# Performance work log

Measured on AMD Instinct MI355X. Metric: run time of the kernel, lower is better.

## Reference

```python
import jax, jax.numpy as jnp
import numpy as np

LN_EPS = 1e-5


def setup_inputs() -> dict:
    key = jax.random.key(0)
    ks = jax.random.split(key, 6)
    B, N, C, H = 8, 4096, 768, 12
    D = C // H
    x = jax.random.normal(ks[0], (B, N, C), dtype=jnp.float32)
    w_qkv = jax.random.normal(ks[1], (3 * C, C), dtype=jnp.float32) * (C ** -0.5)
    w_proj = jax.random.normal(ks[2], (C, C), dtype=jnp.float32) * (C ** -0.5)
    b_proj = jnp.zeros((C,), dtype=jnp.float32)
    # trunc_normal_(std=0.02) approximated by clipped normal
    p1 = jnp.clip(jax.random.normal(ks[3], (H, N), dtype=jnp.float32) * 0.02, -0.04, 0.04)
    p2 = jnp.clip(jax.random.normal(ks[4], (H, N), dtype=jnp.float32) * 0.02, -0.04, 0.04)
    gamma = jnp.ones((D,), dtype=jnp.float32)
    beta = jnp.zeros((D,), dtype=jnp.float32)
    return {"x": x, "w_qkv": w_qkv, "w_proj": w_proj, "b_proj": b_proj,
            "p1": p1, "p2": p2, "gamma": gamma, "beta": beta}


def _layernorm(h, gamma, beta):
    mu = jnp.mean(h, axis=-1, keepdims=True)
    var = jnp.var(h, axis=-1, keepdims=True)
    return (h - mu) * jax.lax.rsqrt(var + LN_EPS) * gamma + beta


def reference(x, w_qkv, w_proj, b_proj, p1, p2, gamma, beta):
    B, N, C = x.shape
    H = p1.shape[0]
    D = C // H
    # qkv projection (no bias): [B,N,3C] -> [3,B,H,N,D]
    qkv = (x @ w_qkv.T).reshape(B, N, 3, H, D).transpose(2, 0, 3, 1, 4)
    q, k, v = qkv[0], qkv[1], qkv[2]
    # weighted k*v reduction over sequence: [B,H,D]
    modulator = jnp.einsum('hn,bhnd->bhd', p2, k * v)
    modulator = _layernorm(modulator, gamma, beta)
    # broadcast modulation back over N: [B,H,N,D]
    modulator = jnp.einsum('hn,bhd->bhnd', p1, modulator)
    out = (q * modulator).transpose(0, 2, 1, 3).reshape(B, N, C)
    return out @ w_proj.T + b_proj
```

## Files before the change

### kernel.cpp

```cpp
#include <hip/hip_runtime.h>
#include <stdint.h>
#include <stddef.h>

#define LN_EPS 1e-5f

typedef __bf16 bf16;
typedef __bf16 bf16x8 __attribute__((ext_vector_type(8)));
typedef __bf16 bf16x4 __attribute__((ext_vector_type(4)));
typedef float f32x4 __attribute__((ext_vector_type(4)));

#define GL16(gp, lp)                                                                   \
  __builtin_amdgcn_global_load_lds((__attribute__((address_space(1))) uint32_t*)(gp),  \
                                   (__attribute__((address_space(3))) uint32_t*)(lp),  \
                                   16, 0, 0)

#define SBAR   asm volatile("s_barrier" ::: "memory")
#define VMW(N) asm volatile("s_waitcnt vmcnt(" #N ")" ::: "memory")
#define LGK(N) asm volatile("s_waitcnt lgkmcnt(" #N ")" ::: "memory")
#define SCB    __builtin_amdgcn_sched_barrier(0)
#define SP1    __builtin_amdgcn_s_setprio(1)
#define SP0    __builtin_amdgcn_s_setprio(0)
#define NOWAIT ((void)0)

#define XV4   6291456
#define WQV4  442368
#define WPV4  147456
__global__ __launch_bounds__(256) void cvt_all(const float* __restrict__ x,
                                               const float* __restrict__ wq,
                                               const float* __restrict__ wp,
                                               bf16* __restrict__ xb,
                                               bf16* __restrict__ wqb,
                                               bf16* __restrict__ wpb) {
  int i = blockIdx.x * 256 + threadIdx.x;
  const float* src; bf16* dst; int off;
  if (i < XV4)              { src = x;  dst = xb;  off = i; }
  else if (i < XV4 + WQV4)  { src = wq; dst = wqb; off = i - XV4; }
  else                      { src = wp; dst = wpb; off = i - (XV4 + WQV4); }
  const float4 v = ((const float4*)src)[off];
  bf16x4 o;
  o[0] = (bf16)v.x; o[1] = (bf16)v.y; o[2] = (bf16)v.z; o[3] = (bf16)v.w;
  ((bf16x4*)dst)[off] = o;
}

#define STAGE_A(T, H) do {                                              \
    bf16* d_ = ldsA + ((((T)&1) << 1) + (H)) * 8192 + tid8;             \
    GL16(pA + (H) * 98304 + (T) * 64, d_);                              \
    GL16(pA + (H) * 98304 + 49152 + (T) * 64, d_ + 4096); } while (0)

#define STAGE_B(T, H) do {                                              \
    bf16* d_ = ldsB + ((((T)&1) << 1) + (H)) * 8192 + tid8;             \
    GL16(pB##H##0 + (T) * 64, d_);                                      \
    GL16(pB##H##1 + (T) * 64, d_ + 4096); } while (0)

#define RD_AQ(D, MQ) do {                                               \
    _Pragma("unroll") for (int mf = 0; mf < 4; ++mf) {                  \
      const int r_ = (MQ) * 64 + mf * 16 + l16;                         \
      const bf16* b_ = ldsA + (((D) << 1) + wm) * 8192 + r_ * 64;       \
      const int x_ = r_ & 7;                                            \
      aF[mf][0] = *(const bf16x8*)(b_ + ((qg ^ x_) << 3));              \
      aF[mf][1] = *(const bf16x8*)(b_ + (((4 + qg) ^ x_) << 3));        \
    } } while (0)

#define RD_BQ(D, NQ, BF) do {                                           \
    _Pragma("unroll") for (int nf = 0; nf < 2; ++nf) {                  \
      const int r_ = hn64 + (NQ) * 32 + nf * 16 + l16;                  \
      const bf16* b_ = ldsB + (((D) << 1) + hb) * 8192 + r_ * 64;       \
      const int x_ = r_ & 7;                                            \
      BF[nf][0] = *(const bf16x8*)(b_ + ((qg ^ x_) << 3));              \
      BF[nf][1] = *(const bf16x8*)(b_ + (((4 + qg) ^ x_) << 3));        \
    } } while (0)

#define MMQ(MQ, NQ, BF) do {                                            \
    _Pragma("unroll") for (int mf = 0; mf < 4; ++mf)                    \
      _Pragma("unroll") for (int nf = 0; nf < 2; ++nf) {                \
        acc[(MQ)*4+mf][(NQ)*2+nf] = __builtin_amdgcn_mfma_f32_16x16x32_bf16( \
            aF[mf][0], BF[nf][0], acc[(MQ)*4+mf][(NQ)*2+nf], 0, 0, 0);  \
        acc[(MQ)*4+mf][(NQ)*2+nf] = __builtin_amdgcn_mfma_f32_16x16x32_bf16( \
            aF[mf][1], BF[nf][1], acc[(MQ)*4+mf][(NQ)*2+nf], 0, 0, 0);  \
      } } while (0)

#define ITER(T, P12, P38, WV4, WV8) do {                                       \
     RD_AQ(0, 0); RD_BQ(0, 0, bF0); if (P12) STAGE_A((T)+1, 0); LGK(8);\
    SBAR; LGK(0); SCB; SP1; MMQ(0, 0, bF0); SP0; SBAR;                         \
     RD_BQ(0, 1, bF1); if (P12) STAGE_A((T)+1, 1);                     \
    SBAR; LGK(0); SCB; SP1; MMQ(0, 1, bF1); SP0; SBAR;                         \
     RD_AQ(0, 1); if (P38) STAGE_B((T)+2, 0);                          \
    SBAR; LGK(0); SCB; SP1; MMQ(1, 0, bF0); SP0; SBAR;                         \
     if (P38) STAGE_B((T)+2, 1);                                       \
    SBAR; LGK(0); SCB; SP1; MMQ(1, 1, bF1); SP0; WV4; SBAR;                    \
     RD_AQ(1, 0); RD_BQ(1, 0, bF0); if (P38) STAGE_A((T)+2, 0); LGK(8);\
    SBAR; LGK(0); SCB; SP1; MMQ(0, 0, bF0); SP0; SBAR;                         \
     RD_BQ(1, 1, bF1); if (P38) STAGE_A((T)+2, 1);                     \
    SBAR; LGK(0); SCB; SP1; MMQ(0, 1, bF1); SP0; SBAR;                         \
     RD_AQ(1, 1); if (P38) STAGE_B((T)+3, 0);                          \
    SBAR; LGK(0); SCB; SP1; MMQ(1, 0, bF0); SP0; SBAR;                         \
     if (P38) STAGE_B((T)+3, 1);                                       \
    SBAR; LGK(0); SCB; SP1; MMQ(1, 1, bF1); SP0; WV8; SBAR;                    \
  } while (0)

__device__ __forceinline__ void gemm256(const bf16* pA,
                                        const bf16* pB00, const bf16* pB01,
                                        const bf16* pB10, const bf16* pB11,
                                        bf16* sh, f32x4 acc[8][4]) {
  const int tid  = threadIdx.x;
  const int lane = tid & 63;
  const int wave = tid >> 6;
  const int wm   = wave >> 2;
  const int wn   = wave & 3;
  const int hb   = wn >> 1;
  const int hn64 = (wn & 1) * 64;
  const int l16  = lane & 15;
  const int qg   = lane >> 4;
  const int tid8 = tid * 8;
  bf16* const ldsA = sh;
  bf16* const ldsB = sh + 32768;
  bf16x8 aF[4][2], bF0[2][2], bF1[2][2];

  STAGE_A(0, 0); STAGE_A(0, 1); STAGE_B(0, 0); STAGE_B(0, 1);
  STAGE_A(1, 0); STAGE_A(1, 1); STAGE_B(1, 0); STAGE_B(1, 1);
  VMW(8);
  SBAR;

  ITER(0, 0, 1, VMW(4), VMW(4));
#pragma unroll 1
  for (int T = 2; T <= 8; T += 2) {
    ITER(T, 1, 1, VMW(4), VMW(4));
  }
  ITER(10, 1, 0, VMW(0), NOWAIT);

  asm volatile("s_waitcnt vmcnt(0) lgkmcnt(0)" ::: "memory");
  __syncthreads();
}

#define QSTAGE_A(T) do {                                          \
    bf16* d_ = qldsA + (((T)&1)) * 8192 + tid8;                   \
    GL16(qA + (T) * 64, d_);                                      \
    GL16(qA + 49152 + (T) * 64, d_ + 4096); } while (0)

#define QSTAGE_B(T, H) do {                                       \
    bf16* d_ = qldsB + ((((T)&1) << 1) + (H)) * 8192 + tid8;      \
    GL16(qB##H##0 + (T) * 64, d_);                                \
    GL16(qB##H##1 + (T) * 64, d_ + 4096); } while (0)

#define QRD_A(D, MQ) do {                                         \
    _Pragma("unroll") for (int mf = 0; mf < 2; ++mf) {            \
      const int r_ = wm * 64 + (MQ) * 32 + mf * 16 + l16;         \
      const bf16* b_ = qldsA + (D) * 8192 + r_ * 64;              \
      const int x_ = r_ & 7;                                      \
      aF[mf][0] = *(const bf16x8*)(b_ + ((qg ^ x_) << 3));        \
      aF[mf][1] = *(const bf16x8*)(b_ + (((4 + qg) ^ x_) << 3));  \
    } } while (0)

#define QRD_B(D, NQ, BF) do {                                     \
    _Pragma("unroll") for (int nf = 0; nf < 2; ++nf) {            \
      const int r_ = hn64 + (NQ) * 32 + nf * 16 + l16;            \
      const bf16* b_ = qldsB + (((D) << 1) + hb) * 8192 + r_ * 64;\
      const int x_ = r_ & 7;                                      \
      BF[nf][0] = *(const bf16x8*)(b_ + ((qg ^ x_) << 3));        \
      BF[nf][1] = *(const bf16x8*)(b_ + (((4 + qg) ^ x_) << 3));  \
    } } while (0)

#define QMM(MQ, NQ, BF) do {                                      \
    _Pragma("unroll") for (int mf = 0; mf < 2; ++mf)              \
      _Pragma("unroll") for (int nf = 0; nf < 2; ++nf) {          \
        acc[(MQ)*2+mf][(NQ)*2+nf] = __builtin_amdgcn_mfma_f32_16x16x32_bf16( \
            aF[mf][0], BF[nf][0], acc[(MQ)*2+mf][(NQ)*2+nf], 0, 0, 0); \
        acc[(MQ)*2+mf][(NQ)*2+nf] = __builtin_amdgcn_mfma_f32_16x16x32_bf16( \
            aF[mf][1], BF[nf][1], acc[(MQ)*2+mf][(NQ)*2+nf], 0, 0, 0); \
      } } while (0)

#define QITER(T, P1, P38, WVp4, WVp8) do {                                     \
     QRD_A(0, 0); QRD_B(0, 0, bF0); if (P1) QSTAGE_A((T)+1);           \
    SBAR; LGK(0); SCB; SP1; QMM(0, 0, bF0); SP0; SBAR;                         \
     QRD_B(0, 1, bF1);                                                 \
    SBAR; LGK(0); SCB; SP1; QMM(0, 1, bF1); SP0; SBAR;                         \
     QRD_A(0, 1); if (P38) QSTAGE_B((T)+2, 0);                         \
    SBAR; LGK(0); SCB; SP1; QMM(1, 0, bF0); SP0; SBAR;                         \
     if (P38) QSTAGE_B((T)+2, 1);                                      \
    SBAR; LGK(0); SCB; SP1; QMM(1, 1, bF1); SP0; WVp4; SBAR;                   \
     QRD_A(1, 0); QRD_B(1, 0, bF0); if (P38) QSTAGE_A((T)+2);          \
    SBAR; LGK(0); SCB; SP1; QMM(0, 0, bF0); SP0; SBAR;                         \
     QRD_B(1, 1, bF1);                                                 \
    SBAR; LGK(0); SCB; SP1; QMM(0, 1, bF1); SP0; SBAR;                         \
     QRD_A(1, 1); if (P38) QSTAGE_B((T)+3, 0);                         \
    SBAR; LGK(0); SCB; SP1; QMM(1, 0, bF0); SP0; SBAR;                         \
     if (P38) QSTAGE_B((T)+3, 1);                                      \
    SBAR; LGK(0); SCB; SP1; QMM(1, 1, bF1); SP0; WVp8; SBAR;                   \
  } while (0)

__device__ __forceinline__ void gemm128x256(const bf16* qA,
                                            const bf16* qB00, const bf16* qB01,
                                            const bf16* qB10, const bf16* qB11,
                                            bf16* sh, f32x4 acc[4][4]) {
  const int tid  = threadIdx.x;
  const int lane = tid & 63;
  const int wave = tid >> 6;
  const int wm   = wave >> 2;
  const int wn   = wave & 3;
  const int hb   = wn >> 1;
  const int hn64 = (wn & 1) * 64;
  const int l16  = lane & 15;
  const int qg   = lane >> 4;
  const int tid8 = tid * 8;
  bf16* const qldsA = sh;
  bf16* const qldsB = sh + 16384;
  bf16x8 aF[2][2], bF0[2][2], bF1[2][2];

  QSTAGE_A(0); QSTAGE_B(0, 0); QSTAGE_B(0, 1);
  QSTAGE_A(1); QSTAGE_B(1, 0); QSTAGE_B(1, 1);
  VMW(6);
  SBAR;

  QITER(0, 0, 1, VMW(4), VMW(4));
#pragma unroll 1
  for (int T = 2; T <= 8; T += 2) {
    QITER(T, 1, 1, VMW(4), VMW(4));
  }
  QITER(10, 1, 0, VMW(0), NOWAIT);

  asm volatile("s_waitcnt vmcnt(0) lgkmcnt(0)" ::: "memory");
  __syncthreads();
}

__global__ __launch_bounds__(512, 2) void kv_gemm_reduce(const bf16* __restrict__ A,
                                                         const bf16* __restrict__ B,
                                                         const float* __restrict__ p2,
                                                         float* __restrict__ partials) {
  __shared__ __align__(16) bf16 sh[65536];
  __shared__ float red2[2][4][2][16];

  const int lin  = blockIdx.y * 6 + blockIdx.x;
  const int xcd  = lin & 7;
  const int j    = lin >> 3;
  const int hh   = j % 6;
  const int mblk = xcd + 8 * (j / 6);
  const int m0   = mblk * 256;
  const int h0   = hh * 2;

  const int tid = threadIdx.x;
  const int tr  = tid >> 3;
  const int tc  = ((tid & 7) ^ ((tid >> 3) & 7)) * 8;
  const bf16* pA = A + (size_t)(m0 + tr) * 768 + tc;
#define WQROW(r) (768 + (((r) >> 4) & 1) * 768 + (h0 + ((r) >> 7)) * 64 + \
                  ((((r) >> 5) & 3) * 16 + ((r) & 15)))
  const bf16* pB00 = B + (size_t)WQROW(tr) * 768 + tc;
  const bf16* pB01 = B + (size_t)WQROW(64 + tr) * 768 + tc;
  const bf16* pB10 = B + (size_t)WQROW(128 + tr) * 768 + tc;
  const bf16* pB11 = B + (size_t)WQROW(192 + tr) * 768 + tc;
#undef WQROW

  f32x4 acc[8][4] = {};
  gemm256(pA, pB00, pB01, pB10, pB11, sh, acc);

  const int lane = tid & 63, wave = tid >> 6;
  const int wm = wave >> 2, wn = wave & 3, l16 = lane & 15, qg = lane >> 4;
  const float* p2h = p2 + (size_t)(h0 + (wn >> 1)) * 4096 + (m0 & 4095) + wm * 128;
  float s0 = 0.f, s1 = 0.f;
#pragma unroll
  for (int ai = 0; ai < 8; ++ai) {
    const float4 w = *(const float4*)(p2h + ai * 16 + qg * 4);
    s0 += w.x * acc[ai][0][0] * acc[ai][1][0] + w.y * acc[ai][0][1] * acc[ai][1][1]
        + w.z * acc[ai][0][2] * acc[ai][1][2] + w.w * acc[ai][0][3] * acc[ai][1][3];
    s1 += w.x * acc[ai][2][0] * acc[ai][3][0] + w.y * acc[ai][2][1] * acc[ai][3][1]
        + w.z * acc[ai][2][2] * acc[ai][3][2] + w.w * acc[ai][2][3] * acc[ai][3][3];
  }
  s0 += __shfl_xor(s0, 16); s0 += __shfl_xor(s0, 32);
  s1 += __shfl_xor(s1, 16); s1 += __shfl_xor(s1, 32);
  if (qg == 0) { red2[wm][wn][0][l16] = s0; red2[wm][wn][1][l16] = s1; }
  __syncthreads();
  if (tid < 128) {
    const int l = tid & 15, jj = (tid >> 4) & 1, wnn = tid >> 5;
    const float v = red2[0][wnn][jj][l] + red2[1][wnn][jj][l];
    const int hx = h0 + (wnn >> 1);
    const int dd = ((wnn & 1) * 2 + jj) * 16 + l;
    partials[((size_t)mblk * 12 + hx) * 64 + dd] = v;
  }
}

__global__ __launch_bounds__(64) void mod_reduce_ln(const float* __restrict__ partials,
                                                    const float* __restrict__ gamma,
                                                    const float* __restrict__ beta,
                                                    float* __restrict__ mod) {
  const int h = blockIdx.x, b = blockIdx.y;
  const int d = threadIdx.x;

  const float* p = partials + ((size_t)(b * 16) * 12 + h) * 64 + d;
  float s = 0.f;
#pragma unroll
  for (int mb = 0; mb < 16; ++mb) s += p[(size_t)mb * 12 * 64];

  float sum = s, sumsq = s * s;
#pragma unroll
  for (int o = 32; o > 0; o >>= 1) {
    sum   += __shfl_xor(sum, o);
    sumsq += __shfl_xor(sumsq, o);
  }
  const float mu  = sum * (1.f / 64.f);
  const float var = sumsq * (1.f / 64.f) - mu * mu;
  const float r   = rsqrtf(var + LN_EPS);
  mod[(b * 12 + h) * 64 + d] = (s - mu) * r * gamma[d] + beta[d];
}

__global__ __launch_bounds__(512, 2) void q_gemm_mod(const bf16* __restrict__ A,
                                                     const bf16* __restrict__ B,
                                                     const float* __restrict__ p1,
                                                     const float* __restrict__ mod,
                                                     bf16* __restrict__ amod) {
  __shared__ __align__(16) bf16 sh[49152];

  const int lin  = blockIdx.y * 3 + blockIdx.x;
  const int xcd  = lin & 7;
  const int j    = lin >> 3;
  const int nblk = j % 3;
  const int mblk = xcd + 8 * (j / 3);
  const int n0   = nblk * 256;
  const int m0   = mblk * 128;

  const int tid = threadIdx.x;
  const int tr  = tid >> 3;
  const int tc  = ((tid & 7) ^ ((tid >> 3) & 7)) * 8;
  const bf16* qA   = A + (size_t)(m0 + tr) * 768 + tc;
  const bf16* qB00 = B + (size_t)(n0 + tr) * 768 + tc;
  const bf16* qB01 = qB00 + (size_t)64 * 768;
  const bf16* qB10 = qB00 + (size_t)128 * 768;
  const bf16* qB11 = qB00 + (size_t)192 * 768;

  f32x4 acc[4][4] = {};
  gemm128x256(qA, qB00, qB01, qB10, qB11, sh, acc);

  const int lane = tid & 63, wave = tid >> 6;
  const int wm = wave >> 2, wn = wave & 3, l16 = lane & 15, qg = lane >> 4;
  const int row0 = m0 + wm * 64 + qg * 4;
  const int col0 = n0 + wn * 64 + l16;
  const int b    = m0 >> 12;
  const int h    = (n0 >> 6) + wn;

  float p1v[4][4];
#pragma unroll
  for (int ai = 0; ai < 4; ++ai)
#pragma unroll
    for (int r = 0; r < 4; ++r)
      p1v[ai][r] = p1[(size_t)h * 4096 + ((row0 + ai * 16 + r) & 4095)];
  float mv[4];
#pragma unroll
  for (int bj = 0; bj < 4; ++bj) mv[bj] = mod[b * 768 + col0 + bj * 16];

#pragma unroll
  for (int ai = 0; ai < 4; ++ai)
#pragma unroll
    for (int bj = 0; bj < 4; ++bj)
#pragma unroll
      for (int r = 0; r < 4; ++r)
        amod[(size_t)(row0 + ai * 16 + r) * 768 + col0 + bj * 16] =
            (bf16)(acc[ai][bj][r] * p1v[ai][r] * mv[bj]);
}

__global__ __launch_bounds__(512, 2) void gemm_proj(const bf16* __restrict__ A,
                                                    const bf16* __restrict__ B,
                                                    const float* __restrict__ bias,
                                                    float* __restrict__ C) {
  __shared__ __align__(16) bf16 sh[49152];

  const int lin  = blockIdx.y * 3 + blockIdx.x;
  const int xcd  = lin & 7;
  const int j    = lin >> 3;
  const int nblk = j % 3;
  const int mblk = xcd + 8 * (j / 3);
  const int n0   = nblk * 256;
  const int m0   = mblk * 128;

  const int tid = threadIdx.x;
  const int tr  = tid >> 3;
  const int tc  = ((tid & 7) ^ ((tid >> 3) & 7)) * 8;
  const bf16* qA   = A + (size_t)(m0 + tr) * 768 + tc;
  const bf16* qB00 = B + (size_t)(n0 + tr) * 768 + tc;
  const bf16* qB01 = qB00 + (size_t)64 * 768;
  const bf16* qB10 = qB00 + (size_t)128 * 768;
  const bf16* qB11 = qB00 + (size_t)192 * 768;

  f32x4 acc[4][4] = {};
  gemm128x256(qA, qB00, qB01, qB10, qB11, sh, acc);

  const int lane = tid & 63, wave = tid >> 6;
  const int wm = wave >> 2, wn = wave & 3, l16 = lane & 15, qg = lane >> 4;
  const int row0 = m0 + wm * 64 + qg * 4;
  const int col0 = n0 + wn * 64 + l16;
#pragma unroll
  for (int bj = 0; bj < 4; ++bj) {
    const int col = col0 + bj * 16;
    const float bv = bias[col];
#pragma unroll
    for (int ai = 0; ai < 4; ++ai)
#pragma unroll
      for (int r = 0; r < 4; ++r)
        C[(size_t)(row0 + ai * 16 + r) * 768 + col] = acc[ai][bj][r] + bv;
  }
}

extern "C" void kernel_launch(void* const* d_in, const int* in_sizes, int n_in,
                              void* d_out, int out_size, void* d_ws, size_t ws_size,
                              hipStream_t stream) {
  (void)in_sizes; (void)n_in; (void)out_size; (void)ws_size;

  const float* x      = (const float*)d_in[0];
  const float* w_qkv  = (const float*)d_in[1];
  const float* w_proj = (const float*)d_in[2];
  const float* b_proj = (const float*)d_in[3];
  const float* p1     = (const float*)d_in[4];
  const float* p2     = (const float*)d_in[5];
  const float* gamma  = (const float*)d_in[6];
  const float* beta   = (const float*)d_in[7];
  float* out = (float*)d_out;

  char* ws = (char*)d_ws;
  bf16*  xb       = (bf16*)(ws + 0);
  bf16*  wqb      = (bf16*)(ws + 50331648);
  bf16*  wpb      = (bf16*)(ws + 53870592);
  bf16*  amod     = (bf16*)(ws + 55050240);
  float* partials = (float*)(ws + 105381888);
  float* mod      = (float*)(ws + 106168320);

  cvt_all<<<26880, 256, 0, stream>>>(x, w_qkv, w_proj, xb, wqb, wpb);

  kv_gemm_reduce<<<dim3(6, 128), 512, 0, stream>>>(xb, wqb, p2, partials);

  mod_reduce_ln<<<dim3(12, 8), 64, 0, stream>>>(partials, gamma, beta, mod);

  q_gemm_mod<<<dim3(3, 256), 512, 0, stream>>>(xb, wqb, p1, mod, amod);

  gemm_proj<<<dim3(3, 256), 512, 0, stream>>>(amod, wpb, b_proj, out);
}
```

Baseline: 355.6 us.

## Replace GEMM cores with shared K=32 double-buffered kernel and fuse LayerNorm

```diff
diff --git a/kernel.cpp b/kernel.cpp
--- a/kernel.cpp
+++ b/kernel.cpp
@@ -31,202 +31,86 @@
                                                bf16* __restrict__ xb,
                                                bf16* __restrict__ wqb,
                                                bf16* __restrict__ wpb) {
-  int i = blockIdx.x * 256 + threadIdx.x;
-  const float* src; bf16* dst; int off;
-  if (i < XV4)              { src = x;  dst = xb;  off = i; }
-  else if (i < XV4 + WQV4)  { src = wq; dst = wqb; off = i - XV4; }
-  else                      { src = wp; dst = wpb; off = i - (XV4 + WQV4); }
-  const float4 v = ((const float4*)src)[off];
-  bf16x4 o;
-  o[0] = (bf16)v.x; o[1] = (bf16)v.y; o[2] = (bf16)v.z; o[3] = (bf16)v.w;
-  ((bf16x4*)dst)[off] = o;
-}
-
-#define STAGE_A(T, H) do {                                              \
-    bf16* d_ = ldsA + ((((T)&1) << 1) + (H)) * 8192 + tid8;             \
-    GL16(pA + (H) * 98304 + (T) * 64, d_);                              \
-    GL16(pA + (H) * 98304 + 49152 + (T) * 64, d_ + 4096); } while (0)
-
-#define STAGE_B(T, H) do {                                              \
-    bf16* d_ = ldsB + ((((T)&1) << 1) + (H)) * 8192 + tid8;             \
-    GL16(pB##H##0 + (T) * 64, d_);                                      \
-    GL16(pB##H##1 + (T) * 64, d_ + 4096); } while (0)
-
-#define RD_AQ(D, MQ) do {                                               \
-    _Pragma("unroll") for (int mf = 0; mf < 4; ++mf) {                  \
-      const int r_ = (MQ) * 64 + mf * 16 + l16;                         \
-      const bf16* b_ = ldsA + (((D) << 1) + wm) * 8192 + r_ * 64;       \
-      const int x_ = r_ & 7;                                            \
-      aF[mf][0] = *(const bf16x8*)(b_ + ((qg ^ x_) << 3));              \
-      aF[mf][1] = *(const bf16x8*)(b_ + (((4 + qg) ^ x_) << 3));        \
+  const int base = blockIdx.x * 256 + threadIdx.x;
+#pragma unroll 1
+  for (int it = 0; it < 16; ++it) {
+    const int i = base + it * 430080;
+    const float* src; bf16* dst; int off;
+    if (i < XV4)              { src = x;  dst = xb;  off = i; }
+    else if (i < XV4 + WQV4)  { src = wq; dst = wqb; off = i - XV4; }
+    else                      { src = wp; dst = wpb; off = i - (XV4 + WQV4); }
+    const float4 v = ((const float4*)src)[off];
+    bf16x4 o;
+    o[0] = (bf16)v.x; o[1] = (bf16)v.y; o[2] = (bf16)v.z; o[3] = (bf16)v.w;
+    ((bf16x4*)dst)[off] = o;
+  }
+}
+
+#define CSTAGE(T, CUR) do {                                    \
+    GL16(cA  + (T) * 32, sh + (CUR) * 12288 + tid8);           \
+    GL16(cB0 + (T) * 32, sh + (CUR) * 12288 + 4096 + tid8);    \
+    GL16(cB1 + (T) * 32, sh + (CUR) * 12288 + 8192 + tid8);    \
+  } while (0)
+
+#define CRD(CUR) do {                                                         \
+    _Pragma("unroll") for (int ff = 0; ff < 4; ++ff) {                        \
+      const int ra = wm * 64 + ff * 16 + l16;                                 \
+      const int rb = wn * 64 + ff * 16 + l16;                                 \
+      aF[ff] = *(const bf16x8*)(sh + (CUR) * 12288 + ra * 32 + coff);         \
+      bF[ff] = *(const bf16x8*)(sh + (CUR) * 12288 + 4096 + rb * 32 + coff);  \
     } } while (0)
 
-#define RD_BQ(D, NQ, BF) do {                                           \
-    _Pragma("unroll") for (int nf = 0; nf < 2; ++nf) {                  \
-      const int r_ = hn64 + (NQ) * 32 + nf * 16 + l16;                  \
-      const bf16* b_ = ldsB + (((D) << 1) + hb) * 8192 + r_ * 64;       \
-      const int x_ = r_ & 7;                                            \
-      BF[nf][0] = *(const bf16x8*)(b_ + ((qg ^ x_) << 3));              \
-      BF[nf][1] = *(const bf16x8*)(b_ + (((4 + qg) ^ x_) << 3));        \
-    } } while (0)
-
-#define MMQ(MQ, NQ, BF) do {                                            \
-    _Pragma("unroll") for (int mf = 0; mf < 4; ++mf)                    \
-      _Pragma("unroll") for (int nf = 0; nf < 2; ++nf) {                \
-        acc[(MQ)*4+mf][(NQ)*2+nf] = __builtin_amdgcn_mfma_f32_16x16x32_bf16( \
-            aF[mf][0], BF[nf][0], acc[(MQ)*4+mf][(NQ)*2+nf], 0, 0, 0);  \
-        acc[(MQ)*4+mf][(NQ)*2+nf] = __builtin_amdgcn_mfma_f32_16x16x32_bf16( \
-            aF[mf][1], BF[nf][1], acc[(MQ)*4+mf][(NQ)*2+nf], 0, 0, 0);  \
-      } } while (0)
-
-#define ITER(T, P12, P38, WV4, WV8) do {                                       \
-     RD_AQ(0, 0); RD_BQ(0, 0, bF0); if (P12) STAGE_A((T)+1, 0); LGK(8);\
-    SBAR; LGK(0); SCB; SP1; MMQ(0, 0, bF0); SP0; SBAR;                         \
-     RD_BQ(0, 1, bF1); if (P12) STAGE_A((T)+1, 1);                     \
-    SBAR; LGK(0); SCB; SP1; MMQ(0, 1, bF1); SP0; SBAR;                         \
-     RD_AQ(0, 1); if (P38) STAGE_B((T)+2, 0);                          \
-    SBAR; LGK(0); SCB; SP1; MMQ(1, 0, bF0); SP0; SBAR;                         \
-     if (P38) STAGE_B((T)+2, 1);                                       \
-    SBAR; LGK(0); SCB; SP1; MMQ(1, 1, bF1); SP0; WV4; SBAR;                    \
-     RD_AQ(1, 0); RD_BQ(1, 0, bF0); if (P38) STAGE_A((T)+2, 0); LGK(8);\
-    SBAR; LGK(0); SCB; SP1; MMQ(0, 0, bF0); SP0; SBAR;                         \
-     RD_BQ(1, 1, bF1); if (P38) STAGE_A((T)+2, 1);                     \
-    SBAR; LGK(0); SCB; SP1; MMQ(0, 1, bF1); SP0; SBAR;                         \
-     RD_AQ(1, 1); if (P38) STAGE_B((T)+3, 0);                          \
-    SBAR; LGK(0); SCB; SP1; MMQ(1, 0, bF0); SP0; SBAR;                         \
-     if (P38) STAGE_B((T)+3, 1);                                       \
-    SBAR; LGK(0); SCB; SP1; MMQ(1, 1, bF1); SP0; WV8; SBAR;                    \
+#define CMM do {                                                              \
+    _Pragma("unroll") for (int ai = 0; ai < 4; ++ai)                          \
+      _Pragma("unroll") for (int bj = 0; bj < 4; ++bj)                        \
+        acc[ai][bj] = __builtin_amdgcn_mfma_f32_16x16x32_bf16(                \
+            aF[ai], bF[bj], acc[ai][bj], 0, 0, 0);                            \
   } while (0)
 
-__device__ __forceinline__ void gemm256(const bf16* pA,
-                                        const bf16* pB00, const bf16* pB01,
-                                        const bf16* pB10, const bf16* pB11,
-                                        bf16* sh, f32x4 acc[8][4]) {
+#define CITER(CUR, STG, WAIT) do {  \
+    CRD(CUR);                       \
+    LGK(0); SCB;                    \
+    SBAR;                           \
+    STG;                            \
+    SP1; CMM; SP0;                  \
+    WAIT;                           \
+    SBAR;                           \
+  } while (0)
+
+__device__ __forceinline__ void gemmC(const bf16* cA, const bf16* cB0,
+                                      const bf16* cB1, bf16* sh,
+                                      f32x4 acc[4][4]) {
   const int tid  = threadIdx.x;
   const int lane = tid & 63;
   const int wave = tid >> 6;
   const int wm   = wave >> 2;
   const int wn   = wave & 3;
-  const int hb   = wn >> 1;
-  const int hn64 = (wn & 1) * 64;
   const int l16  = lane & 15;
   const int qg   = lane >> 4;
   const int tid8 = tid * 8;
-  bf16* const ldsA = sh;
-  bf16* const ldsB = sh + 32768;
-  bf16x8 aF[4][2], bF0[2][2], bF1[2][2];
-
-  STAGE_A(0, 0); STAGE_A(0, 1); STAGE_B(0, 0); STAGE_B(0, 1);
-  STAGE_A(1, 0); STAGE_A(1, 1); STAGE_B(1, 0); STAGE_B(1, 1);
-  VMW(8);
+  const int coff = ((qg ^ ((l16 >> 1) & 3)) << 3);
+  bf16x8 aF[4], bF[4];
+
+  CSTAGE(0, 0); CSTAGE(1, 1);
+  VMW(3);
   SBAR;
 
-  ITER(0, 0, 1, VMW(4), VMW(4));
 #pragma unroll 1
-  for (int T = 2; T <= 8; T += 2) {
-    ITER(T, 1, 1, VMW(4), VMW(4));
-  }
-  ITER(10, 1, 0, VMW(0), NOWAIT);
-
+  for (int t = 0; t < 22; t += 2) {
+    CITER(0, CSTAGE(t + 2, 0), VMW(3));
+    CITER(1, CSTAGE(t + 3, 1), VMW(3));
+  }
+  CITER(0, NOWAIT, VMW(0));
+  CITER(1, NOWAIT, NOWAIT);
   asm volatile("s_waitcnt vmcnt(0) lgkmcnt(0)" ::: "memory");
   __syncthreads();
 }
 
-#define QSTAGE_A(T) do {                                          \
-    bf16* d_ = qldsA + (((T)&1)) * 8192 + tid8;                   \
-    GL16(qA + (T) * 64, d_);                                      \
-    GL16(qA + 49152 + (T) * 64, d_ + 4096); } while (0)
-
-#define QSTAGE_B(T, H) do {                                       \
-    bf16* d_ = qldsB + ((((T)&1) << 1) + (H)) * 8192 + tid8;      \
-    GL16(qB##H##0 + (T) * 64, d_);                                \
-    GL16(qB##H##1 + (T) * 64, d_ + 4096); } while (0)
-
-#define QRD_A(D, MQ) do {                                         \
-    _Pragma("unroll") for (int mf = 0; mf < 2; ++mf) {            \
-      const int r_ = wm * 64 + (MQ) * 32 + mf * 16 + l16;         \
-      const bf16* b_ = qldsA + (D) * 8192 + r_ * 64;              \
-      const int x_ = r_ & 7;                                      \
-      aF[mf][0] = *(const bf16x8*)(b_ + ((qg ^ x_) << 3));        \
-      aF[mf][1] = *(const bf16x8*)(b_ + (((4 + qg) ^ x_) << 3));  \
-    } } while (0)
-
-#define QRD_B(D, NQ, BF) do {                                     \
-    _Pragma("unroll") for (int nf = 0; nf < 2; ++nf) {            \
-      const int r_ = hn64 + (NQ) * 32 + nf * 16 + l16;            \
-      const bf16* b_ = qldsB + (((D) << 1) + hb) * 8192 + r_ * 64;\
-      const int x_ = r_ & 7;                                      \
-      BF[nf][0] = *(const bf16x8*)(b_ + ((qg ^ x_) << 3));        \
-      BF[nf][1] = *(const bf16x8*)(b_ + (((4 + qg) ^ x_) << 3));  \
-    } } while (0)
-
-#define QMM(MQ, NQ, BF) do {                                      \
-    _Pragma("unroll") for (int mf = 0; mf < 2; ++mf)              \
-      _Pragma("unroll") for (int nf = 0; nf < 2; ++nf) {          \
-        acc[(MQ)*2+mf][(NQ)*2+nf] = __builtin_amdgcn_mfma_f32_16x16x32_bf16( \
-            aF[mf][0], BF[nf][0], acc[(MQ)*2+mf][(NQ)*2+nf], 0, 0, 0); \
-        acc[(MQ)*2+mf][(NQ)*2+nf] = __builtin_amdgcn_mfma_f32_16x16x32_bf16( \
-            aF[mf][1], BF[nf][1], acc[(MQ)*2+mf][(NQ)*2+nf], 0, 0, 0); \
-      } } while (0)
-
-#define QITER(T, P1, P38, WVp4, WVp8) do {                                     \
-     QRD_A(0, 0); QRD_B(0, 0, bF0); if (P1) QSTAGE_A((T)+1);           \
-    SBAR; LGK(0); SCB; SP1; QMM(0, 0, bF0); SP0; SBAR;                         \
-     QRD_B(0, 1, bF1);                                                 \
-    SBAR; LGK(0); SCB; SP1; QMM(0, 1, bF1); SP0; SBAR;                         \
-     QRD_A(0, 1); if (P38) QSTAGE_B((T)+2, 0);                         \
-    SBAR; LGK(0); SCB; SP1; QMM(1, 0, bF0); SP0; SBAR;                         \
-     if (P38) QSTAGE_B((T)+2, 1);                                      \
-    SBAR; LGK(0); SCB; SP1; QMM(1, 1, bF1); SP0; WVp4; SBAR;                   \
-     QRD_A(1, 0); QRD_B(1, 0, bF0); if (P38) QSTAGE_A((T)+2);          \
-    SBAR; LGK(0); SCB; SP1; QMM(0, 0, bF0); SP0; SBAR;                         \
-     QRD_B(1, 1, bF1);                                                 \
-    SBAR; LGK(0); SCB; SP1; QMM(0, 1, bF1); SP0; SBAR;                         \
-     QRD_A(1, 1); if (P38) QSTAGE_B((T)+3, 0);                         \
-    SBAR; LGK(0); SCB; SP1; QMM(1, 0, bF0); SP0; SBAR;                         \
-     if (P38) QSTAGE_B((T)+3, 1);                                      \
-    SBAR; LGK(0); SCB; SP1; QMM(1, 1, bF1); SP0; WVp8; SBAR;                   \
-  } while (0)
-
-__device__ __forceinline__ void gemm128x256(const bf16* qA,
-                                            const bf16* qB00, const bf16* qB01,
-                                            const bf16* qB10, const bf16* qB11,
-                                            bf16* sh, f32x4 acc[4][4]) {
-  const int tid  = threadIdx.x;
-  const int lane = tid & 63;
-  const int wave = tid >> 6;
-  const int wm   = wave >> 2;
-  const int wn   = wave & 3;
-  const int hb   = wn >> 1;
-  const int hn64 = (wn & 1) * 64;
-  const int l16  = lane & 15;
-  const int qg   = lane >> 4;
-  const int tid8 = tid * 8;
-  bf16* const qldsA = sh;
-  bf16* const qldsB = sh + 16384;
-  bf16x8 aF[2][2], bF0[2][2], bF1[2][2];
-
-  QSTAGE_A(0); QSTAGE_B(0, 0); QSTAGE_B(0, 1);
-  QSTAGE_A(1); QSTAGE_B(1, 0); QSTAGE_B(1, 1);
-  VMW(6);
-  SBAR;
-
-  QITER(0, 0, 1, VMW(4), VMW(4));
-#pragma unroll 1
-  for (int T = 2; T <= 8; T += 2) {
-    QITER(T, 1, 1, VMW(4), VMW(4));
-  }
-  QITER(10, 1, 0, VMW(0), NOWAIT);
-
-  asm volatile("s_waitcnt vmcnt(0) lgkmcnt(0)" ::: "memory");
-  __syncthreads();
-}
-
-__global__ __launch_bounds__(512, 2) void kv_gemm_reduce(const bf16* __restrict__ A,
+__global__ __launch_bounds__(512, 4) void kv_gemm_reduce(const bf16* __restrict__ A,
                                                          const bf16* __restrict__ B,
                                                          const float* __restrict__ p2,
                                                          float* __restrict__ partials) {
-  __shared__ __align__(16) bf16 sh[65536];
+  __shared__ __align__(16) bf16 sh[24576];
   __shared__ float red2[2][4][2][16];
 
   const int lin  = blockIdx.y * 6 + blockIdx.x;
@@ -234,30 +118,28 @@
   const int j    = lin >> 3;
   const int hh   = j % 6;
   const int mblk = xcd + 8 * (j / 6);
-  const int m0   = mblk * 256;
+  const int m0   = mblk * 128;
   const int h0   = hh * 2;
 
   const int tid = threadIdx.x;
-  const int tr  = tid >> 3;
-  const int tc  = ((tid & 7) ^ ((tid >> 3) & 7)) * 8;
-  const bf16* pA = A + (size_t)(m0 + tr) * 768 + tc;
+  const int tr  = tid >> 2;
+  const int tc  = ((tid & 3) ^ ((tid >> 3) & 3)) * 8;
+  const bf16* cA = A + (size_t)(m0 + tr) * 768 + tc;
 #define WQROW(r) (768 + (((r) >> 4) & 1) * 768 + (h0 + ((r) >> 7)) * 64 + \
                   ((((r) >> 5) & 3) * 16 + ((r) & 15)))
-  const bf16* pB00 = B + (size_t)WQROW(tr) * 768 + tc;
-  const bf16* pB01 = B + (size_t)WQROW(64 + tr) * 768 + tc;
-  const bf16* pB10 = B + (size_t)WQROW(128 + tr) * 768 + tc;
-  const bf16* pB11 = B + (size_t)WQROW(192 + tr) * 768 + tc;
+  const bf16* cB0 = B + (size_t)WQROW(tr) * 768 + tc;
+  const bf16* cB1 = B + (size_t)WQROW(128 + tr) * 768 + tc;
 #undef WQROW
 
-  f32x4 acc[8][4] = {};
-  gemm256(pA, pB00, pB01, pB10, pB11, sh, acc);
+  f32x4 acc[4][4] = {};
+  gemmC(cA, cB0, cB1, sh, acc);
 
   const int lane = tid & 63, wave = tid >> 6;
   const int wm = wave >> 2, wn = wave & 3, l16 = lane & 15, qg = lane >> 4;
-  const float* p2h = p2 + (size_t)(h0 + (wn >> 1)) * 4096 + (m0 & 4095) + wm * 128;
+  const float* p2h = p2 + (size_t)(h0 + (wn >> 1)) * 4096 + (m0 & 4095) + wm * 64;
   float s0 = 0.f, s1 = 0.f;
 #pragma unroll
-  for (int ai = 0; ai < 8; ++ai) {
+  for (int ai = 0; ai < 4; ++ai) {
     const float4 w = *(const float4*)(p2h + ai * 16 + qg * 4);
     s0 += w.x * acc[ai][0][0] * acc[ai][1][0] + w.y * acc[ai][0][1] * acc[ai][1][1]
         + w.z * acc[ai][0][2] * acc[ai][1][2] + w.w * acc[ai][0][3] * acc[ai][1][3];
@@ -277,36 +159,15 @@
   }
 }
 
-__global__ __launch_bounds__(64) void mod_reduce_ln(const float* __restrict__ partials,
-                                                    const float* __restrict__ gamma,
-                                                    const float* __restrict__ beta,
-                                                    float* __restrict__ mod) {
-  const int h = blockIdx.x, b = blockIdx.y;
-  const int d = threadIdx.x;
-
-  const float* p = partials + ((size_t)(b * 16) * 12 + h) * 64 + d;
-  float s = 0.f;
-#pragma unroll
-  for (int mb = 0; mb < 16; ++mb) s += p[(size_t)mb * 12 * 64];
-
-  float sum = s, sumsq = s * s;
-#pragma unroll
-  for (int o = 32; o > 0; o >>= 1) {
-    sum   += __shfl_xor(sum, o);
-    sumsq += __shfl_xor(sumsq, o);
-  }
-  const float mu  = sum * (1.f / 64.f);
-  const float var = sumsq * (1.f / 64.f) - mu * mu;
-  const float r   = rsqrtf(var + LN_EPS);
-  mod[(b * 12 + h) * 64 + d] = (s - mu) * r * gamma[d] + beta[d];
-}
-
-__global__ __launch_bounds__(512, 2) void q_gemm_mod(const bf16* __restrict__ A,
+__global__ __launch_bounds__(512, 4) void q_gemm_mod(const bf16* __restrict__ A,
                                                      const bf16* __restrict__ B,
                                                      const float* __restrict__ p1,
-                                                     const float* __restrict__ mod,
+                                                     const float* __restrict__ partials,
+                                                     const float* __restrict__ gamma,
+                                                     const float* __restrict__ beta,
                                                      bf16* __restrict__ amod) {
-  __shared__ __align__(16) bf16 sh[49152];
+  __shared__ __align__(16) bf16 sh[24576];
+  __shared__ float mod_s[4][64];
 
   const int lin  = blockIdx.y * 3 + blockIdx.x;
   const int xcd  = lin & 7;
@@ -315,25 +176,41 @@
   const int mblk = xcd + 8 * (j / 3);
   const int n0   = nblk * 256;
   const int m0   = mblk * 128;
+  const int b    = mblk >> 5;
+  const int h0q  = nblk * 4;
 
   const int tid = threadIdx.x;
-  const int tr  = tid >> 3;
-  const int tc  = ((tid & 7) ^ ((tid >> 3) & 7)) * 8;
-  const bf16* qA   = A + (size_t)(m0 + tr) * 768 + tc;
-  const bf16* qB00 = B + (size_t)(n0 + tr) * 768 + tc;
-  const bf16* qB01 = qB00 + (size_t)64 * 768;
-  const bf16* qB10 = qB00 + (size_t)128 * 768;
-  const bf16* qB11 = qB00 + (size_t)192 * 768;
+  if (tid < 256) {
+    const int hl = tid >> 6, d = tid & 63;
+    const float* p = partials + ((size_t)(b * 32) * 12 + h0q + hl) * 64 + d;
+    float s = 0.f;
+#pragma unroll
+    for (int mb = 0; mb < 32; ++mb) s += p[(size_t)mb * 12 * 64];
+    float sum = s, sumsq = s * s;
+#pragma unroll
+    for (int o = 32; o > 0; o >>= 1) {
+      sum += __shfl_xor(sum, o); sumsq += __shfl_xor(sumsq, o);
+    }
+    const float mu  = sum * (1.f / 64.f);
+    const float var = sumsq * (1.f / 64.f) - mu * mu;
+    mod_s[hl][d] = (s - mu) * rsqrtf(var + LN_EPS) * gamma[d] + beta[d];
+  }
+  __syncthreads();
+
+  const int tr = tid >> 2;
+  const int tc = ((tid & 3) ^ ((tid >> 3) & 3)) * 8;
+  const bf16* cA  = A + (size_t)(m0 + tr) * 768 + tc;
+  const bf16* cB0 = B + (size_t)(n0 + tr) * 768 + tc;
+  const bf16* cB1 = B + (size_t)(n0 + 128 + tr) * 768 + tc;
 
   f32x4 acc[4][4] = {};
-  gemm128x256(qA, qB00, qB01, qB10, qB11, sh, acc);
+  gemmC(cA, cB0, cB1, sh, acc);
 
   const int lane = tid & 63, wave = tid >> 6;
   const int wm = wave >> 2, wn = wave & 3, l16 = lane & 15, qg = lane >> 4;
   const int row0 = m0 + wm * 64 + qg * 4;
   const int col0 = n0 + wn * 64 + l16;
-  const int b    = m0 >> 12;
-  const int h    = (n0 >> 6) + wn;
+  const int h    = h0q + wn;
 
   float p1v[4][4];
 #pragma unroll
@@ -343,7 +220,7 @@
       p1v[ai][r] = p1[(size_t)h * 4096 + ((row0 + ai * 16 + r) & 4095)];
   float mv[4];
 #pragma unroll
-  for (int bj = 0; bj < 4; ++bj) mv[bj] = mod[b * 768 + col0 + bj * 16];
+  for (int bj = 0; bj < 4; ++bj) mv[bj] = mod_s[wn][bj * 16 + l16];
 
 #pragma unroll
   for (int ai = 0; ai < 4; ++ai)
@@ -355,11 +232,11 @@
             (bf16)(acc[ai][bj][r] * p1v[ai][r] * mv[bj]);
 }
 
-__global__ __launch_bounds__(512, 2) void gemm_proj(const bf16* __restrict__ A,
+__global__ __launch_bounds__(512, 4) void gemm_proj(const bf16* __restrict__ A,
                                                     const bf16* __restrict__ B,
                                                     const float* __restrict__ bias,
                                                     float* __restrict__ C) {
-  __shared__ __align__(16) bf16 sh[49152];
+  __shared__ __align__(16) bf16 sh[24576];
 
   const int lin  = blockIdx.y * 3 + blockIdx.x;
   const int xcd  = lin & 7;
@@ -370,16 +247,14 @@
   const int m0   = mblk * 128;
 
   const int tid = threadIdx.x;
-  const int tr  = tid >> 3;
-  const int tc  = ((tid & 7) ^ ((tid >> 3) & 7)) * 8;
-  const bf16* qA   = A + (size_t)(m0 + tr) * 768 + tc;
-  const bf16* qB00 = B + (size_t)(n0 + tr) * 768 + tc;
-  const bf16* qB01 = qB00 + (size_t)64 * 768;
-  const bf16* qB10 = qB00 + (size_t)128 * 768;
-  const bf16* qB11 = qB00 + (size_t)192 * 768;
+  const int tr  = tid >> 2;
+  const int tc  = ((tid & 3) ^ ((tid >> 3) & 3)) * 8;
+  const bf16* cA  = A + (size_t)(m0 + tr) * 768 + tc;
+  const bf16* cB0 = B + (size_t)(n0 + tr) * 768 + tc;
+  const bf16* cB1 = B + (size_t)(n0 + 128 + tr) * 768 + tc;
 
   f32x4 acc[4][4] = {};
-  gemm128x256(qA, qB00, qB01, qB10, qB11, sh, acc);
+  gemmC(cA, cB0, cB1, sh, acc);
 
   const int lane = tid & 63, wave = tid >> 6;
   const int wm = wave >> 2, wn = wave & 3, l16 = lane & 15, qg = lane >> 4;
@@ -418,15 +293,13 @@
   bf16*  wpb      = (bf16*)(ws + 53870592);
   bf16*  amod     = (bf16*)(ws + 55050240);
   float* partials = (float*)(ws + 105381888);
-  float* mod      = (float*)(ws + 106168320);
-
-  cvt_all<<<26880, 256, 0, stream>>>(x, w_qkv, w_proj, xb, wqb, wpb);
-
-  kv_gemm_reduce<<<dim3(6, 128), 512, 0, stream>>>(xb, wqb, p2, partials);
-
-  mod_reduce_ln<<<dim3(12, 8), 64, 0, stream>>>(partials, gamma, beta, mod);
-
-  q_gemm_mod<<<dim3(3, 256), 512, 0, stream>>>(xb, wqb, p1, mod, amod);
+
+  cvt_all<<<1680, 256, 0, stream>>>(x, w_qkv, w_proj, xb, wqb, wpb);
+
+  kv_gemm_reduce<<<dim3(6, 256), 512, 0, stream>>>(xb, wqb, p2, partials);
+
+  q_gemm_mod<<<dim3(3, 256), 512, 0, stream>>>(xb, wqb, p1, partials,
+                                               gamma, beta, amod);
 
   gemm_proj<<<dim3(3, 256), 512, 0, stream>>>(amod, wpb, b_proj, out);
 }
```

Result: no change. 357.7 us (+0.6%).
